# Kernel tuning notes

Measured on AMD Instinct MI355X. Metric: run time of the kernel, lower is better.

The kernel has to match this reference:

```python
import jax, jax.numpy as jnp
import numpy as np

DN = ('NCDHW', 'OIDHW', 'NCDHW')

def conv3d(x, w, b):
    y = jax.lax.conv_general_dilated(x, w, window_strides=(1, 1, 1),
                                     padding=[(1, 1)] * 3, dimension_numbers=DN)
    return y + b[None, :, None, None, None]

def setup_inputs() -> dict:
    key = jax.random.key(0)
    ks = jax.random.split(key, 9)
    B, Cin, D, H, W = 2, 64, 8, 16, 16
    s = 0.05
    return {
        'x': jax.random.normal(ks[0], (B, Cin, D, H, W), jnp.float32),
        'w_key': jax.random.normal(ks[1], (32, Cin, 3, 3, 3), jnp.float32) * s,
        'b_key': jax.random.normal(ks[2], (32,), jnp.float32) * s,
        'w_query': jax.random.normal(ks[3], (32, Cin, 3, 3, 3), jnp.float32) * s,
        'b_query': jax.random.normal(ks[4], (32,), jnp.float32) * s,
        'w_value': jax.random.normal(ks[5], (32, Cin, 3, 3, 3), jnp.float32) * s,
        'b_value': jax.random.normal(ks[6], (32,), jnp.float32) * s,
        'w_alter': jax.random.normal(ks[7], (64, 32, 3, 3, 3), jnp.float32) * s,
        'b_alter': jax.random.normal(ks[8], (64,), jnp.float32) * s,
    }

def reference(x, w_key, b_key, w_query, b_query, w_value, b_value, w_alter, b_alter):
    k = conv3d(x, w_key, b_key)      # [B,32,D,H,W]
    q = conv3d(x, w_query, b_query)
    v = conv3d(x, w_value, b_value)
    B, C, D, H, W = k.shape
    N = D * H * W
    kf = k.reshape(B, C, N)
    qf = q.reshape(B, C, N)
    vf = v.reshape(B, C, N)
    qp = jnp.transpose(qf, (1, 2, 0))  # [C,N,B]
    kp = jnp.transpose(kf, (1, 0, 2))  # [C,B,N]
    vp = jnp.transpose(vf, (1, 2, 0))  # [C,N,B]
    # attn: [C,N,N]; torch softmax over dim=1 (the query/row N axis)
    attn = jax.nn.softmax(jnp.einsum('cnb,cbm->cnm', qp, kp), axis=1)
    out = jnp.einsum('cnm,cmb->cnb', attn, vp)  # [C,N,B]
    # torch .view reinterprets the contiguous [C,N,B] buffer as [B,C,D,H,W]
    out = out.reshape(B, C, D, H, W)
    out = conv3d(out, w_alter, b_alter)  # [B,64,D,H,W]
    return x + out
```

## Files before the change

kernel.cpp:

```cpp
#include <hip/hip_runtime.h>

#define BB 2
#define CIN 64
#define CQ 32
#define DD 8
#define HH 16
#define WWW 16
#define NN 2048
#define NHW 256
#define COUT 64

#define XPLANE 324
#define CI_OUT 8

#define QROWS 18
#define QCOLS 20
#define QPLANE (QROWS * QCOLS)
#define QCI 4

#define NPART 8
#define LOG2E 1.44269504088896340736f

__device__ __forceinline__ float fast_exp2(float x) {
#if __has_builtin(__builtin_amdgcn_exp2f)
    return __builtin_amdgcn_exp2f(x);
#else
    return exp2f(x);
#endif
}

__global__ __launch_bounds__(256) void init_kernel(
    const float* __restrict__ bk, const float* __restrict__ bq, const float* __restrict__ bv,
    const float* __restrict__ ba, const float* __restrict__ x,
    float* __restrict__ kout, float* __restrict__ qout, float* __restrict__ vout,
    float* __restrict__ out)
{
    int i = blockIdx.x * 256 + threadIdx.x;
    if (i < BB * CQ * NN) {
        int co = (i >> 11) & 31;
        kout[i] = bk[co];
        qout[i] = bq[co];
        vout[i] = bv[co];
    } else {
        int j = i - BB * CQ * NN;
        int co = (j >> 11) & 63;
        out[j] = x[j] + ba[co];
    }
}

__global__ __launch_bounds__(256, 2) void conv_qkv_kernel(
    const float* __restrict__ x,
    const float* __restrict__ wk, const float* __restrict__ wq, const float* __restrict__ wv,
    float* __restrict__ kout, float* __restrict__ qout, float* __restrict__ vout)
{
    int bid   = blockIdx.x;
    int split = bid >> 7;
    int inner = bid & 127;
    int co    = inner & 31;
    int dq    = (inner >> 5) & 1;
    int b     = inner >> 6;
    int ci0   = split << 4;
    int d0    = dq << 2;

    __shared__ float xl[QCI * 6 * QPLANE];
    __shared__ float tl[1024];

    int tid = threadIdx.x;
    int hw = tid >> 4;
    int ww = tid & 15;
    int wr = (hw + 1) * QCOLS + (ww + 1);
    int pn  = tid >> 6;
    int rem = tid & 63;
    int h   = rem >> 2;
    int wqi = rem & 3;

    const float* xb = x + ((size_t)b * CIN + ci0) * NN;

    float r[QCI * 6];
    #pragma unroll
    for (int p = 0; p < 6; ++p) {
        int dd = d0 - 1 + p;
        if (dd >= 0 && dd < DD) {
            #pragma unroll
            for (int cl = 0; cl < QCI; ++cl)
                r[cl * 6 + p] = xb[(size_t)cl * NN + dd * NHW + tid];
        }
    }
    for (int i = tid; i < QCI * 6 * QPLANE; i += 256) xl[i] = 0.f;
    __syncthreads();
    #pragma unroll
    for (int p = 0; p < 6; ++p) {
        int dd = d0 - 1 + p;
        if (dd >= 0 && dd < DD) {
            #pragma unroll
            for (int cl = 0; cl < QCI; ++cl)
                xl[cl * 6 * QPLANE + p * QPLANE + wr] = r[cl * 6 + p];
        }
    }

    float acc[3][4];
    #pragma unroll
    for (int s = 0; s < 3; ++s)
        #pragma unroll
        for (int o = 0; o < 4; ++o) acc[s][o] = 0.f;

    #pragma unroll 1
    for (int ph = 0; ph < 4; ++ph) {
        __syncthreads();
        if (ph < 3) {
            #pragma unroll
            for (int p = 0; p < 6; ++p) {
                int dd = d0 - 1 + p;
                if (dd >= 0 && dd < DD) {
                    #pragma unroll
                    for (int cl = 0; cl < QCI; ++cl)
                        r[cl * 6 + p] = xb[(size_t)((ph + 1) * QCI + cl) * NN + dd * NHW + tid];
                }
            }
        }

        #pragma unroll 1
        for (int cl = 0; cl < QCI; ++cl) {
            int ci = ci0 + ph * QCI + cl;
            const float* wk0 = wk + ((size_t)co * CIN + ci) * 27;
            const float* wq0 = wq + ((size_t)co * CIN + ci) * 27;
            const float* wv0 = wv + ((size_t)co * CIN + ci) * 27;
            const float* xp  = xl + cl * 6 * QPLANE + pn * QPLANE + h * QCOLS + wqi * 4;

            #pragma unroll
            for (int kd = 0; kd < 3; ++kd) {
                float ws[3][9];
                #pragma unroll
                for (int j = 0; j < 9; ++j) {
                    int t = kd * 9 + j;
                    ws[0][j] = wk0[t]; ws[1][j] = wq0[t]; ws[2][j] = wv0[t];
                }
                #pragma unroll
                for (int kh = 0; kh < 3; ++kh) {
                    const float* xr = xp + kd * QPLANE + kh * QCOLS;
                    float4 xa  = *(const float4*)xr;
                    float2 xb2 = *(const float2*)(xr + 4);
                    float xw[6] = {xa.x, xa.y, xa.z, xa.w, xb2.x, xb2.y};
                    #pragma unroll
                    for (int kw = 0; kw < 3; ++kw) {
                        int t = kh * 3 + kw;
                        #pragma unroll
                        for (int o = 0; o < 4; ++o) {
                            float xv = xw[o + kw];
                            acc[0][o] = fmaf(ws[0][t], xv, acc[0][o]);
                            acc[1][o] = fmaf(ws[1][t], xv, acc[1][o]);
                            acc[2][o] = fmaf(ws[2][t], xv, acc[2][o]);
                        }
                    }
                }
            }
        }

        __syncthreads();
        if (ph < 3) {
            #pragma unroll
            for (int p = 0; p < 6; ++p) {
                int dd = d0 - 1 + p;
                if (dd >= 0 && dd < DD) {
                    #pragma unroll
                    for (int cl = 0; cl < QCI; ++cl)
                        xl[cl * 6 * QPLANE + p * QPLANE + wr] = r[cl * 6 + p];
                }
            }
        }
    }

    size_t base = ((size_t)b * CQ + co) * NN + d0 * NHW;
    int wloc = pn * 256 + h * 16 + wqi * 4;
    #define EMIT_SET(S, BUF) { \
        __syncthreads(); \
        float4 f; f.x = acc[S][0]; f.y = acc[S][1]; f.z = acc[S][2]; f.w = acc[S][3]; \
        *(float4*)&tl[wloc] = f; \
        __syncthreads(); \
        unsafeAtomicAdd(&BUF[base + 0 * NHW + tid], tl[tid]); \
        unsafeAtomicAdd(&BUF[base + 1 * NHW + tid], tl[tid + 256]); \
        unsafeAtomicAdd(&BUF[base + 2 * NHW + tid], tl[tid + 512]); \
        unsafeAtomicAdd(&BUF[base + 3 * NHW + tid], tl[tid + 768]); }
    EMIT_SET(0, kout)
    EMIT_SET(1, qout)
    EMIT_SET(2, vout)
    #undef EMIT_SET
}

__global__ __launch_bounds__(256) void mz_partial_kernel(
    const float* __restrict__ kbuf, const float* __restrict__ qbuf,
    float* __restrict__ pmax, float* __restrict__ psum)
{
    int bid = blockIdx.x;
    int nchunk = bid & 7;
    int mtile  = (bid >> 3) & 3;
    int c      = bid >> 5;

    __shared__ float q0l[256], q1l[256];
    int tid = threadIdx.x;
    int n0 = nchunk * 256;
    if (tid < 64) {
        float4 v = ((const float4*)(qbuf + (size_t)c * NN + n0))[tid];
        v.x *= LOG2E; v.y *= LOG2E; v.z *= LOG2E; v.w *= LOG2E;
        ((float4*)q0l)[tid] = v;
    } else if (tid < 128) {
        float4 v = ((const float4*)(qbuf + (size_t)(CQ + c) * NN + n0))[tid - 64];
        v.x *= LOG2E; v.y *= LOG2E; v.z *= LOG2E; v.w *= LOG2E;
        ((float4*)q1l)[tid - 64] = v;
    }
    __syncthreads();

    int m = mtile * 512 + tid * 2;
    float2 k0 = *(const float2*)(kbuf + (size_t)c * NN + m);
    float2 k1 = *(const float2*)(kbuf + (size_t)(CQ + c) * NN + m);

    const float4* q0v = (const float4*)q0l;
    const float4* q1v = (const float4*)q1l;

    float mxa = -1e30f, mxb = -1e30f;
    #pragma unroll 4
    for (int i = 0; i < 64; ++i) {
        float4 a = q0v[i], b4 = q1v[i];
        float sa0 = fmaf(k0.x, a.x, k1.x * b4.x);
        float sa1 = fmaf(k0.x, a.y, k1.x * b4.y);
        float sa2 = fmaf(k0.x, a.z, k1.x * b4.z);
        float sa3 = fmaf(k0.x, a.w, k1.x * b4.w);
        mxa = fmaxf(mxa, fmaxf(fmaxf(sa0, sa1), fmaxf(sa2, sa3)));
        float sb0 = fmaf(k0.y, a.x, k1.y * b4.x);
        float sb1 = fmaf(k0.y, a.y, k1.y * b4.y);
        float sb2 = fmaf(k0.y, a.z, k1.y * b4.z);
        float sb3 = fmaf(k0.y, a.w, k1.y * b4.w);
        mxb = fmaxf(mxb, fmaxf(fmaxf(sb0, sb1), fmaxf(sb2, sb3)));
    }

    float nma = -mxa, nmb = -mxb;
    float za = 0.f, zb = 0.f;
    #pragma unroll 4
    for (int i = 0; i < 64; ++i) {
        float4 a = q0v[i], b4 = q1v[i];
        za += fast_exp2(fmaf(k0.x, a.x, fmaf(k1.x, b4.x, nma)))
            + fast_exp2(fmaf(k0.x, a.y, fmaf(k1.x, b4.y, nma)))
            + fast_exp2(fmaf(k0.x, a.z, fmaf(k1.x, b4.z, nma)))
            + fast_exp2(fmaf(k0.x, a.w, fmaf(k1.x, b4.w, nma)));
        zb += fast_exp2(fmaf(k0.y, a.x, fmaf(k1.y, b4.x, nmb)))
            + fast_exp2(fmaf(k0.y, a.y, fmaf(k1.y, b4.y, nmb)))
            + fast_exp2(fmaf(k0.y, a.z, fmaf(k1.y, b4.z, nmb)))
            + fast_exp2(fmaf(k0.y, a.w, fmaf(k1.y, b4.w, nmb)));
    }
    size_t o = ((size_t)c * NPART + nchunk) * NN + m;
    float2 rm; rm.x = mxa; rm.y = mxb;
    float2 rz; rz.x = za;  rz.y = zb;
    *(float2*)(pmax + o) = rm;
    *(float2*)(psum + o) = rz;
}

__global__ __launch_bounds__(256) void att_partial_kernel(
    const float* __restrict__ kbuf, const float* __restrict__ qbuf,
    const float* __restrict__ vbuf,
    const float* __restrict__ pmax, const float* __restrict__ psum,
    float* __restrict__ parts)
{
    int bid = blockIdx.x;
    int mchunk = bid & 7;
    int ntile  = (bid >> 3) & 3;
    int c      = bid >> 5;

    __shared__ float k0l[256], k1l[256], vz0l[256], vz1l[256], nMl[256];
    int tid = threadIdx.x;
    {
        int m = mchunk * 256 + tid;
        float pj[NPART];
        float M = -1e30f;
        #pragma unroll
        for (int j = 0; j < NPART; ++j) {
            pj[j] = pmax[((size_t)c * NPART + j) * NN + m];
            M = fmaxf(M, pj[j]);
        }
        float z = 0.f;
        #pragma unroll
        for (int j = 0; j < NPART; ++j)
            z += psum[((size_t)c * NPART + j) * NN + m] * fast_exp2(pj[j] - M);
        float rz = 1.f / z;
        k0l[tid]  = kbuf[(size_t)c * NN + m];
        k1l[tid]  = kbuf[(size_t)(CQ + c) * NN + m];
        vz0l[tid] = vbuf[(size_t)c * NN + m] * rz;
        vz1l[tid] = vbuf[(size_t)(CQ + c) * NN + m] * rz;
        nMl[tid]  = -M;
    }
    __syncthreads();

    int n = ntile * 512 + tid * 2;
    float2 q0 = *(const float2*)(qbuf + (size_t)c * NN + n);
    float2 q1 = *(const float2*)(qbuf + (size_t)(CQ + c) * NN + n);
    q0.x *= LOG2E; q0.y *= LOG2E;
    q1.x *= LOG2E; q1.y *= LOG2E;

    const float4* k0v = (const float4*)k0l;
    const float4* k1v = (const float4*)k1l;
    const float4* v0v = (const float4*)vz0l;
    const float4* v1v = (const float4*)vz1l;
    const float4* nMv = (const float4*)nMl;

    float a00 = 0.f, a01 = 0.f;
    float a10 = 0.f, a11 = 0.f;

    #pragma unroll 2
    for (int i = 0; i < 64; ++i) {
        float4 kk0 = k0v[i], kk1 = k1v[i], w0 = v0v[i], w1 = v1v[i], nm = nMv[i];
        #define ATTS(KX,K1X,W0X,W1X,NMX) { \
            float e0 = fast_exp2(fmaf(q0.x, KX, fmaf(q1.x, K1X, NMX))); \
            float e1 = fast_exp2(fmaf(q0.y, KX, fmaf(q1.y, K1X, NMX))); \
            a00 = fmaf(e0, W0X, a00); a10 = fmaf(e0, W1X, a10); \
            a01 = fmaf(e1, W0X, a01); a11 = fmaf(e1, W1X, a11); }
        ATTS(kk0.x, kk1.x, w0.x, w1.x, nm.x)
        ATTS(kk0.y, kk1.y, w0.y, w1.y, nm.y)
        ATTS(kk0.z, kk1.z, w0.z, w1.z, nm.z)
        ATTS(kk0.w, kk1.w, w0.w, w1.w, nm.w)
        #undef ATTS
    }

    float* dst = parts + (size_t)mchunk * (CQ * NN * BB);
    size_t base = ((size_t)c * NN + n) * BB;
    float4 r0; r0.x = a00; r0.y = a10; r0.z = a01; r0.w = a11;
    *(float4*)(dst + base) = r0;
}

__global__ __launch_bounds__(256) void combine_kernel(
    const float* __restrict__ parts, float* __restrict__ ybuf)
{
    int i = blockIdx.x * 256 + threadIdx.x;
    float4 s = ((const float4*)parts)[i];
    #pragma unroll
    for (int j = 1; j < NPART; ++j) {
        float4 p = ((const float4*)(parts + (size_t)j * (CQ * NN * BB)))[i];
        s.x += p.x; s.y += p.y; s.z += p.z; s.w += p.w;
    }
    ((float4*)ybuf)[i] = s;
}

__global__ __launch_bounds__(256, 4) void conv_out_kernel(
    const float* __restrict__ ybuf,
    const float* __restrict__ wa,
    float* __restrict__ out)
{
    int bid   = blockIdx.x;
    int split = bid & 3;
    int cog   = (bid >> 2) & 15;
    int d     = (bid >> 6) & 7;
    int b     = bid >> 9;
    int co0   = cog << 2;
    int ci0   = split << 3;

    __shared__ float yl[CI_OUT * 3 * XPLANE];

    int tid = threadIdx.x;
    int h  = tid >> 4;
    int w  = tid & 15;
    int wr = (h + 1) * 18 + (w + 1);
    int rb = h * 18 + w;

    const float* yb = ybuf + ((size_t)b * CQ + ci0) * NN;

    float r[CI_OUT * 3];
    #pragma unroll
    for (int kd = 0; kd < 3; ++kd) {
        int dd = d + kd - 1;
        bool ok = (dd >= 0) && (dd < DD);
        #pragma unroll
        for (int cc = 0; cc < CI_OUT; ++cc)
            r[cc * 3 + kd] = ok ? yb[(size_t)cc * NN + dd * NHW + tid] : 0.f;
    }
    for (int i = tid; i < CI_OUT * 3 * XPLANE; i += 256) yl[i] = 0.f;
    __syncthreads();
    #pragma unroll
    for (int j = 0; j < CI_OUT * 3; ++j)
        yl[j * XPLANE + wr] = r[j];
    __syncthreads();

    float a0 = 0.f, a1 = 0.f, a2 = 0.f, a3 = 0.f;

    for (int cc = 0; cc < CI_OUT; ++cc) {
        int ci = ci0 + cc;
        const float* w0 = wa + ((size_t)(co0 + 0) * CQ + ci) * 27;
        const float* w1 = wa + ((size_t)(co0 + 1) * CQ + ci) * 27;
        const float* w2 = wa + ((size_t)(co0 + 2) * CQ + ci) * 27;
        const float* w3 = wa + ((size_t)(co0 + 3) * CQ + ci) * 27;
        const float* yp = yl + cc * 3 * XPLANE + rb;
        #pragma unroll
        for (int kd = 0; kd < 3; ++kd) {
            int dd = d + kd - 1;
            if (dd < 0 || dd >= DD) continue;
            #pragma unroll
            for (int kh = 0; kh < 3; ++kh) {
                #pragma unroll
                for (int kw = 0; kw < 3; ++kw) {
                    float yv = yp[kd * XPLANE + kh * 18 + kw];
                    int t = kd * 9 + kh * 3 + kw;
                    a0 = fmaf(yv, w0[t], a0);
                    a1 = fmaf(yv, w1[t], a1);
                    a2 = fmaf(yv, w2[t], a2);
                    a3 = fmaf(yv, w3[t], a3);
                }
            }
        }
    }

    size_t o = ((size_t)b * COUT + co0) * NN + d * NHW + tid;
    unsafeAtomicAdd(&out[o],          a0);
    unsafeAtomicAdd(&out[o + NN],     a1);
    unsafeAtomicAdd(&out[o + 2 * NN], a2);
    unsafeAtomicAdd(&out[o + 3 * NN], a3);
}

extern "C" void kernel_launch(void* const* d_in, const int* in_sizes, int n_in,
                              void* d_out, int out_size, void* d_ws, size_t ws_size,
                              hipStream_t stream) {
    const float* x  = (const float*)d_in[0];
    const float* wk = (const float*)d_in[1];
    const float* bk = (const float*)d_in[2];
    const float* wq = (const float*)d_in[3];
    const float* bq = (const float*)d_in[4];
    const float* wv = (const float*)d_in[5];
    const float* bv = (const float*)d_in[6];
    const float* wa = (const float*)d_in[7];
    const float* ba = (const float*)d_in[8];
    float* out = (float*)d_out;

    float* ws   = (float*)d_ws;
    float* kbuf = ws;
    float* qbuf = kbuf + BB * CQ * NN;
    float* vbuf = qbuf + BB * CQ * NN;
    float* pmax = vbuf + BB * CQ * NN;
    float* psum = pmax + CQ * NPART * NN;
    float* parts = psum + CQ * NPART * NN;
    float* ybuf = kbuf;

    init_kernel<<<1536, 256, 0, stream>>>(bk, bq, bv, ba, x, kbuf, qbuf, vbuf, out);
    conv_qkv_kernel<<<512, 256, 0, stream>>>(x, wk, wq, wv, kbuf, qbuf, vbuf);
    mz_partial_kernel<<<1024, 256, 0, stream>>>(kbuf, qbuf, pmax, psum);
    att_partial_kernel<<<1024, 256, 0, stream>>>(kbuf, qbuf, vbuf, pmax, psum, parts);
    combine_kernel<<<128, 256, 0, stream>>>(parts, ybuf);
    conv_out_kernel<<<1024, 256, 0, stream>>>(ybuf, wa, out);
}
```

Baseline: 102.0 us.

## Replace exact softmax max pass with Cauchy-Schwarz bound and atomic reductions

```diff
diff --git a/kernel.cpp b/kernel.cpp
--- a/kernel.cpp
+++ b/kernel.cpp
@@ -18,7 +18,6 @@
 #define QPLANE (QROWS * QCOLS)
 #define QCI 4
 
-#define NPART 8
 #define LOG2E 1.44269504088896340736f
 
 __device__ __forceinline__ float fast_exp2(float x) {
@@ -33,7 +32,7 @@
     const float* __restrict__ bk, const float* __restrict__ bq, const float* __restrict__ bv,
     const float* __restrict__ ba, const float* __restrict__ x,
     float* __restrict__ kout, float* __restrict__ qout, float* __restrict__ vout,
-    float* __restrict__ out)
+    float* __restrict__ out, float* __restrict__ zbuf, float* __restrict__ ybuf)
 {
     int i = blockIdx.x * 256 + threadIdx.x;
     if (i < BB * CQ * NN) {
@@ -41,10 +40,14 @@
         kout[i] = bk[co];
         qout[i] = bq[co];
         vout[i] = bv[co];
-    } else {
+    } else if (i < 3 * BB * CQ * NN) {
         int j = i - BB * CQ * NN;
         int co = (j >> 11) & 63;
         out[j] = x[j] + ba[co];
+    } else if (i < 3 * BB * CQ * NN + CQ * NN) {
+        zbuf[i - 3 * BB * CQ * NN] = 0.f;
+    } else {
+        ybuf[i - 3 * BB * CQ * NN - CQ * NN] = 0.f;
     }
 }
 
@@ -63,7 +66,7 @@
     int d0    = dq << 2;
 
     __shared__ float xl[QCI * 6 * QPLANE];
-    __shared__ float tl[1024];
+    __shared__ float tl[3 * 1024];
 
     int tid = threadIdx.x;
     int hw = tid >> 4;
@@ -172,29 +175,50 @@
 
     size_t base = ((size_t)b * CQ + co) * NN + d0 * NHW;
     int wloc = pn * 256 + h * 16 + wqi * 4;
-    #define EMIT_SET(S, BUF) { \
-        __syncthreads(); \
-        float4 f; f.x = acc[S][0]; f.y = acc[S][1]; f.z = acc[S][2]; f.w = acc[S][3]; \
-        *(float4*)&tl[wloc] = f; \
-        __syncthreads(); \
-        unsafeAtomicAdd(&BUF[base + 0 * NHW + tid], tl[tid]); \
-        unsafeAtomicAdd(&BUF[base + 1 * NHW + tid], tl[tid + 256]); \
-        unsafeAtomicAdd(&BUF[base + 2 * NHW + tid], tl[tid + 512]); \
-        unsafeAtomicAdd(&BUF[base + 3 * NHW + tid], tl[tid + 768]); }
-    EMIT_SET(0, kout)
-    EMIT_SET(1, qout)
-    EMIT_SET(2, vout)
-    #undef EMIT_SET
+    __syncthreads();
+    {
+        float4 f0; f0.x = acc[0][0]; f0.y = acc[0][1]; f0.z = acc[0][2]; f0.w = acc[0][3];
+        float4 f1; f1.x = acc[1][0]; f1.y = acc[1][1]; f1.z = acc[1][2]; f1.w = acc[1][3];
+        float4 f2; f2.x = acc[2][0]; f2.y = acc[2][1]; f2.z = acc[2][2]; f2.w = acc[2][3];
+        *(float4*)&tl[wloc]        = f0;
+        *(float4*)&tl[1024 + wloc] = f1;
+        *(float4*)&tl[2048 + wloc] = f2;
+    }
+    __syncthreads();
+    #pragma unroll
+    for (int p = 0; p < 4; ++p) {
+        unsafeAtomicAdd(&kout[base + p * NHW + tid], tl[p * 256 + tid]);
+        unsafeAtomicAdd(&qout[base + p * NHW + tid], tl[1024 + p * 256 + tid]);
+        unsafeAtomicAdd(&vout[base + p * NHW + tid], tl[2048 + p * 256 + tid]);
+    }
+}
+
+__global__ __launch_bounds__(256) void qmax_kernel(
+    const float* __restrict__ qbuf, float* __restrict__ mq)
+{
+    int row = blockIdx.x;
+    int tid = threadIdx.x;
+    const float4* q = (const float4*)(qbuf + (size_t)row * NN);
+    float4 v0 = q[tid], v1 = q[tid + 256];
+    float mx = fmaxf(fmaxf(fmaxf(fabsf(v0.x), fabsf(v0.y)), fmaxf(fabsf(v0.z), fabsf(v0.w))),
+                     fmaxf(fmaxf(fabsf(v1.x), fabsf(v1.y)), fmaxf(fabsf(v1.z), fabsf(v1.w))));
+    #pragma unroll
+    for (int off = 32; off; off >>= 1)
+        mx = fmaxf(mx, __shfl_down(mx, off, 64));
+    __shared__ float red[4];
+    if ((tid & 63) == 0) red[tid >> 6] = mx;
+    __syncthreads();
+    if (tid == 0) mq[row] = fmaxf(fmaxf(red[0], red[1]), fmaxf(red[2], red[3]));
 }
 
 __global__ __launch_bounds__(256) void mz_partial_kernel(
     const float* __restrict__ kbuf, const float* __restrict__ qbuf,
-    float* __restrict__ pmax, float* __restrict__ psum)
+    const float* __restrict__ mq, float* __restrict__ zbuf)
 {
     int bid = blockIdx.x;
-    int nchunk = bid & 7;
-    int mtile  = (bid >> 3) & 3;
-    int c      = bid >> 5;
+    int nchunk = bid >> 7;
+    int c      = (bid >> 2) & 31;
+    int mtile  = bid & 3;
 
     __shared__ float q0l[256], q1l[256];
     int tid = threadIdx.x;
@@ -213,27 +237,14 @@
     int m = mtile * 512 + tid * 2;
     float2 k0 = *(const float2*)(kbuf + (size_t)c * NN + m);
     float2 k1 = *(const float2*)(kbuf + (size_t)(CQ + c) * NN + m);
+    float mq0 = mq[c], mq1 = mq[CQ + c];
+
+    float nma = -LOG2E * fmaf(fabsf(k0.x), mq0, fabsf(k1.x) * mq1);
+    float nmb = -LOG2E * fmaf(fabsf(k0.y), mq0, fabsf(k1.y) * mq1);
 
     const float4* q0v = (const float4*)q0l;
     const float4* q1v = (const float4*)q1l;
 
-    float mxa = -1e30f, mxb = -1e30f;
-    #pragma unroll 4
-    for (int i = 0; i < 64; ++i) {
-        float4 a = q0v[i], b4 = q1v[i];
-        float sa0 = fmaf(k0.x, a.x, k1.x * b4.x);
-        float sa1 = fmaf(k0.x, a.y, k1.x * b4.y);
-        float sa2 = fmaf(k0.x, a.z, k1.x * b4.z);
-        float sa3 = fmaf(k0.x, a.w, k1.x * b4.w);
-        mxa = fmaxf(mxa, fmaxf(fmaxf(sa0, sa1), fmaxf(sa2, sa3)));
-        float sb0 = fmaf(k0.y, a.x, k1.y * b4.x);
-        float sb1 = fmaf(k0.y, a.y, k1.y * b4.y);
-        float sb2 = fmaf(k0.y, a.z, k1.y * b4.z);
-        float sb3 = fmaf(k0.y, a.w, k1.y * b4.w);
-        mxb = fmaxf(mxb, fmaxf(fmaxf(sb0, sb1), fmaxf(sb2, sb3)));
-    }
-
-    float nma = -mxa, nmb = -mxb;
     float za = 0.f, zb = 0.f;
     #pragma unroll 4
     for (int i = 0; i < 64; ++i) {
@@ -247,45 +258,34 @@
             + fast_exp2(fmaf(k0.y, a.z, fmaf(k1.y, b4.z, nmb)))
             + fast_exp2(fmaf(k0.y, a.w, fmaf(k1.y, b4.w, nmb)));
     }
-    size_t o = ((size_t)c * NPART + nchunk) * NN + m;
-    float2 rm; rm.x = mxa; rm.y = mxb;
-    float2 rz; rz.x = za;  rz.y = zb;
-    *(float2*)(pmax + o) = rm;
-    *(float2*)(psum + o) = rz;
+    unsafeAtomicAdd(&zbuf[(size_t)c * NN + m],     za);
+    unsafeAtomicAdd(&zbuf[(size_t)c * NN + m + 1], zb);
 }
 
 __global__ __launch_bounds__(256) void att_partial_kernel(
     const float* __restrict__ kbuf, const float* __restrict__ qbuf,
     const float* __restrict__ vbuf,
-    const float* __restrict__ pmax, const float* __restrict__ psum,
-    float* __restrict__ parts)
+    const float* __restrict__ mq, const float* __restrict__ zbuf,
+    float* __restrict__ ybuf)
 {
     int bid = blockIdx.x;
-    int mchunk = bid & 7;
-    int ntile  = (bid >> 3) & 3;
-    int c      = bid >> 5;
+    int mchunk = bid >> 7;
+    int c      = (bid >> 2) & 31;
+    int ntile  = bid & 3;
 
     __shared__ float k0l[256], k1l[256], vz0l[256], vz1l[256], nMl[256];
     int tid = threadIdx.x;
     {
         int m = mchunk * 256 + tid;
-        float pj[NPART];
-        float M = -1e30f;
-        #pragma unroll
-        for (int j = 0; j < NPART; ++j) {
-            pj[j] = pmax[((size_t)c * NPART + j) * NN + m];
-            M = fmaxf(M, pj[j]);
-        }
-        float z = 0.f;
-        #pragma unroll
-        for (int j = 0; j < NPART; ++j)
-            z += psum[((size_t)c * NPART + j) * NN + m] * fast_exp2(pj[j] - M);
-        float rz = 1.f / z;
-        k0l[tid]  = kbuf[(size_t)c * NN + m];
-        k1l[tid]  = kbuf[(size_t)(CQ + c) * NN + m];
+        float k0 = kbuf[(size_t)c * NN + m];
+        float k1 = kbuf[(size_t)(CQ + c) * NN + m];
+        float mq0 = mq[c], mq1 = mq[CQ + c];
+        float rz = 1.f / zbuf[(size_t)c * NN + m];
+        k0l[tid]  = k0;
+        k1l[tid]  = k1;
         vz0l[tid] = vbuf[(size_t)c * NN + m] * rz;
         vz1l[tid] = vbuf[(size_t)(CQ + c) * NN + m] * rz;
-        nMl[tid]  = -M;
+        nMl[tid]  = -LOG2E * fmaf(fabsf(k0), mq0, fabsf(k1) * mq1);
     }
     __syncthreads();
 
@@ -319,23 +319,11 @@
         #undef ATTS
     }
 
-    float* dst = parts + (size_t)mchunk * (CQ * NN * BB);
     size_t base = ((size_t)c * NN + n) * BB;
-    float4 r0; r0.x = a00; r0.y = a10; r0.z = a01; r0.w = a11;
-    *(float4*)(dst + base) = r0;
-}
-
-__global__ __launch_bounds__(256) void combine_kernel(
-    const float* __restrict__ parts, float* __restrict__ ybuf)
-{
-    int i = blockIdx.x * 256 + threadIdx.x;
-    float4 s = ((const float4*)parts)[i];
-    #pragma unroll
-    for (int j = 1; j < NPART; ++j) {
-        float4 p = ((const float4*)(parts + (size_t)j * (CQ * NN * BB)))[i];
-        s.x += p.x; s.y += p.y; s.z += p.z; s.w += p.w;
-    }
-    ((float4*)ybuf)[i] = s;
+    unsafeAtomicAdd(&ybuf[base + 0], a00);
+    unsafeAtomicAdd(&ybuf[base + 1], a10);
+    unsafeAtomicAdd(&ybuf[base + 2], a01);
+    unsafeAtomicAdd(&ybuf[base + 3], a11);
 }
 
 __global__ __launch_bounds__(256, 4) void conv_out_kernel(
@@ -430,15 +418,14 @@
     float* kbuf = ws;
     float* qbuf = kbuf + BB * CQ * NN;
     float* vbuf = qbuf + BB * CQ * NN;
-    float* pmax = vbuf + BB * CQ * NN;
-    float* psum = pmax + CQ * NPART * NN;
-    float* parts = psum + CQ * NPART * NN;
-    float* ybuf = kbuf;
-
-    init_kernel<<<1536, 256, 0, stream>>>(bk, bq, bv, ba, x, kbuf, qbuf, vbuf, out);
+    float* zbuf = vbuf + BB * CQ * NN;
+    float* ybuf = zbuf + CQ * NN;
+    float* mqb  = ybuf + BB * CQ * NN;
+
+    init_kernel<<<2304, 256, 0, stream>>>(bk, bq, bv, ba, x, kbuf, qbuf, vbuf, out, zbuf, ybuf);
     conv_qkv_kernel<<<512, 256, 0, stream>>>(x, wk, wq, wv, kbuf, qbuf, vbuf);
-    mz_partial_kernel<<<1024, 256, 0, stream>>>(kbuf, qbuf, pmax, psum);
-    att_partial_kernel<<<1024, 256, 0, stream>>>(kbuf, qbuf, vbuf, pmax, psum, parts);
-    combine_kernel<<<128, 256, 0, stream>>>(parts, ybuf);
+    qmax_kernel<<<64, 256, 0, stream>>>(qbuf, mqb);
+    mz_partial_kernel<<<1024, 256, 0, stream>>>(kbuf, qbuf, mqb, zbuf);
+    att_partial_kernel<<<1024, 256, 0, stream>>>(kbuf, qbuf, vbuf, mqb, zbuf, ybuf);
     conv_out_kernel<<<1024, 256, 0, stream>>>(ybuf, wa, out);
 }
```

Measured after the change: 96.63 us. 5.2% less time.
